# Kernel tuning notes

Measured on AMD Instinct MI355X. Metric: run time of the kernel, lower is better.

Reference implementation:

```python
import jax, jax.numpy as jnp
import numpy as np

HIDDEN = 1024
NUM_HEADS = 16
HEAD_DIM = HIDDEN // NUM_HEADS
ROPE_THETA = 10000.0


def rope_tables(seq_len, head_dim, theta):
    inv_freq = 1.0 / theta ** (jnp.arange(0, head_dim, 2, dtype=jnp.float32) / head_dim)
    pos = jnp.arange(seq_len, dtype=jnp.float32)
    freqs = jnp.outer(pos, inv_freq)  # [S, hd/2]
    return jnp.cos(freqs), jnp.sin(freqs)


def apply_rope(x, cos, sin):
    # x: [B, nh, S, hd]; cos/sin: [S, hd/2]
    x1, x2 = jnp.split(x, 2, axis=-1)
    return jnp.concatenate([x1 * cos - x2 * sin, x2 * cos + x1 * sin], axis=-1)


def setup_inputs() -> dict:
    key = jax.random.key(0)
    k1, k2, k3 = jax.random.split(key, 3)
    B, S = 2, 2048
    hidden_states = jax.random.normal(k1, (B, S, HIDDEN), dtype=jnp.float32)
    # nn.Linear stores weight as [out, in]; y = x @ W.T
    Wqkv = jax.random.normal(k2, (3 * HIDDEN, HIDDEN), dtype=jnp.float32) * (HIDDEN ** -0.5)
    Wo = jax.random.normal(k3, (HIDDEN, HIDDEN), dtype=jnp.float32) * (HIDDEN ** -0.5)
    return {"hidden_states": hidden_states, "Wqkv": Wqkv, "Wo": Wo}


def reference(hidden_states, Wqkv, Wo):
    B, S, H = hidden_states.shape
    qkv = hidden_states @ Wqkv.T  # [B, S, 3H]
    qkv = qkv.reshape(B, S, 3, NUM_HEADS, HEAD_DIM)
    q, k, v = jnp.moveaxis(qkv, 2, 0)  # each [B, S, nh, hd]
    q = jnp.transpose(q, (0, 2, 1, 3))  # [B, nh, S, hd]
    k = jnp.transpose(k, (0, 2, 1, 3))
    v = jnp.transpose(v, (0, 2, 1, 3))
    cos, sin = rope_tables(S, HEAD_DIM, ROPE_THETA)
    q = apply_rope(q, cos, sin)
    k = apply_rope(k, cos, sin)
    scale = 1.0 / jnp.sqrt(jnp.asarray(HEAD_DIM, dtype=q.dtype))
    scores = jnp.einsum("bhqd,bhkd->bhqk", q, k) * scale
    causal = jnp.tril(jnp.ones((S, S), dtype=bool))
    scores = jnp.where(causal, scores, jnp.finfo(scores.dtype).min)
    attn = jax.nn.softmax(scores, axis=-1)
    out = jnp.einsum("bhqk,bhkd->bhqd", attn, v)  # [B, nh, S, hd]
    out = jnp.transpose(out, (0, 2, 1, 3)).reshape(B, S, H)
    return out @ Wo.T
```

## Files before the change

kernel.cpp:

```cpp
#include <hip/hip_runtime.h>
#include <hip/hip_bf16.h>
#include <math.h>

typedef __bf16 bf16_t;
typedef __attribute__((ext_vector_type(8))) __bf16 bf16x8;
typedef __attribute__((ext_vector_type(4))) float f32x4;
typedef __attribute__((ext_vector_type(16))) float f32x16;
typedef __attribute__((ext_vector_type(4))) unsigned u32x4;

#define AS1(p) ((__attribute__((address_space(1))) void*)(p))
#define AS3(p) ((__attribute__((address_space(3))) void*)(p))

__device__ inline unsigned pkbf(float a, float b) {
  bf16_t x = (bf16_t)a, y = (bf16_t)b;
  return (unsigned)__builtin_bit_cast(unsigned short, x) |
         ((unsigned)__builtin_bit_cast(unsigned short, y) << 16);
}
__device__ inline f32x16 zero16() {
  f32x16 z;
#pragma unroll
  for (int r = 0; r < 16; ++r) z[r] = 0.f;
  return z;
}

__device__ inline void cvt8(const float* __restrict__ in, bf16_t* __restrict__ out, int i) {
  const float4* p = (const float4*)in;
  float4 a = p[2 * i], b = p[2 * i + 1];
  bf16x8 o;
  o[0] = (bf16_t)a.x; o[1] = (bf16_t)a.y; o[2] = (bf16_t)a.z; o[3] = (bf16_t)a.w;
  o[4] = (bf16_t)b.x; o[5] = (bf16_t)b.y; o[6] = (bf16_t)b.z; o[7] = (bf16_t)b.w;
  ((bf16x8*)out)[i] = o;
}

__global__ __launch_bounds__(256)
void prep_all(const float* __restrict__ hid, const float* __restrict__ wqkv,
              const float* __restrict__ wo, bf16_t* __restrict__ hidb,
              bf16_t* __restrict__ wqkvb, bf16_t* __restrict__ wob,
              float* __restrict__ cosb, float* __restrict__ sinb) {
  const int bid = blockIdx.x, tid = threadIdx.x;
  if (bid < 2048) {
    cvt8(hid, hidb, bid * 256 + tid);
  } else if (bid < 3584) {
    cvt8(wqkv, wqkvb, (bid - 2048) * 256 + tid);
  } else if (bid < 4096) {
    cvt8(wo, wob, (bid - 3584) * 256 + tid);
  } else {
    int t = (bid - 4096) * 256 + tid;
    int s = t >> 5, i = t & 31;
    float inv = powf(10000.0f, -(float)i / 32.0f);
    float sv, cv;
    sincosf((float)s * inv, &sv, &cv);
    cosb[t] = cv;
    sinb[t] = sv;
  }
}

#define GSTAGE32(KT, BUF)                                                                  \
  do {                                                                                     \
    const int k0_ = (KT) << 5;                                                             \
    const int ar_ = tid >> 2, ac_ = (tid & 3) * 8;                                         \
    __builtin_amdgcn_global_load_lds(AS1(A + (size_t)(m0 + ar_) * K + k0_ + ac_),          \
                                     AS3(&lA[BUF][ar_ * 32 + ac_]), 16, 0, 0);             \
    __builtin_amdgcn_global_load_lds(AS1(A + (size_t)(m0 + 64 + ar_) * K + k0_ + ac_),     \
                                     AS3(&lA[BUF][(64 + ar_) * 32 + ac_]), 16, 0, 0);      \
    __builtin_amdgcn_global_load_lds(AS1(B + (size_t)(n0 + ar_) * K + k0_ + ac_),          \
                                     AS3(&lB[BUF][ar_ * 32 + ac_]), 16, 0, 0);             \
    __builtin_amdgcn_global_load_lds(AS1(B + (size_t)(n0 + 64 + ar_) * K + k0_ + ac_),     \
                                     AS3(&lB[BUF][(64 + ar_) * 32 + ac_]), 16, 0, 0);      \
  } while (0)

__global__ __launch_bounds__(256, 3)
void gemm_qkv(const bf16_t* __restrict__ A, const bf16_t* __restrict__ B,
              bf16_t* __restrict__ qkv, bf16_t* __restrict__ Kp,
              const float* __restrict__ cosb, const float* __restrict__ sinb) {
  __shared__ __align__(16) bf16_t lA[3][128 * 32];
  __shared__ __align__(16) bf16_t lB[3][128 * 32];
  const int K = 1024;
  const int tid = threadIdx.x;
  const int wid = tid >> 6, lane = tid & 63;
  const int lr = lane & 15, lg = lane >> 4;
  const int nwg = gridDim.x * gridDim.y;
  int lin = blockIdx.y * gridDim.x + blockIdx.x;
  lin = (lin & 7) * (nwg >> 3) + (lin >> 3);
  const int m0 = (lin / gridDim.x) * 128, n0 = (lin % gridDim.x) * 128;
  const int wm = (wid >> 1) * 64, wn = (wid & 1) * 64;
  f32x4 acc[4][4];
#pragma unroll
  for (int i = 0; i < 4; ++i)
#pragma unroll
    for (int j = 0; j < 4; ++j) acc[i][j] = f32x4{0.f, 0.f, 0.f, 0.f};

  const int nk = 32;
  GSTAGE32(0, 0);
  GSTAGE32(1, 1);
  int cbuf = 0;
  for (int kt = 0; kt < nk; ++kt) {
    if (kt + 2 < nk) {
      const int sb = cbuf == 0 ? 2 : cbuf - 1;
      GSTAGE32(kt + 2, sb);
      asm volatile("s_waitcnt vmcnt(8)" ::: "memory");
    } else if (kt + 1 < nk) {
      asm volatile("s_waitcnt vmcnt(4)" ::: "memory");
    } else {
      asm volatile("s_waitcnt vmcnt(0)" ::: "memory");
    }
    __builtin_amdgcn_s_barrier();
    {
      bf16x8 af[4], bfr[4];
#pragma unroll
      for (int i = 0; i < 4; ++i) {
        af[i]  = *(const bf16x8*)&lA[cbuf][(wm + i * 16 + lr) * 32 + lg * 8];
        bfr[i] = *(const bf16x8*)&lB[cbuf][(wn + i * 16 + lr) * 32 + lg * 8];
      }
#pragma unroll
      for (int i = 0; i < 4; ++i)
#pragma unroll
        for (int j = 0; j < 4; ++j)
          acc[i][j] = __builtin_amdgcn_mfma_f32_16x16x32_bf16(af[i], bfr[j], acc[i][j], 0, 0, 0);
    }
    __builtin_amdgcn_s_barrier();
    cbuf = cbuf == 2 ? 0 : cbuf + 1;
  }
  const int sec = n0 >> 10;
  const int hcol = ((n0 + wn) & 1023) >> 6;
  if (sec == 2) {
#pragma unroll
    for (int i = 0; i < 4; ++i) {
      int token0 = m0 + wm + i * 16 + lg * 4;
      int bb = token0 >> 11;
      int t = (token0 & 2047) >> 6;
      int kv0 = token0 & 63;
      bf16_t* vd = qkv + ((size_t)(bb * 2048 + t * 64)) * 3072 + 2048 + hcol * 64;
#pragma unroll
      for (int j = 0; j < 4; ++j) {
        int d = j * 16 + lr;
        uint2 w;
        w.x = pkbf(acc[i][j][0], acc[i][j][1]);
        w.y = pkbf(acc[i][j][2], acc[i][j][3]);
        *(uint2*)(vd + (size_t)d * 3072 + (((kv0 >> 3) ^ (d & 7)) * 8) + (kv0 & 7)) = w;
      }
    }
  } else {
    const float SC = sec ? 1.0f : 0.125f * 1.4426950408889634f;
#pragma unroll
    for (int i = 0; i < 4; ++i)
#pragma unroll
      for (int r = 0; r < 4; ++r) {
        int token = m0 + wm + i * 16 + lg * 4 + r;
        int s = token & 2047;
#pragma unroll
        for (int j = 0; j < 2; ++j) {
          int f = j * 16 + lr;
          float cv = cosb[s * 32 + f], sv = sinb[s * 32 + f];
          float x1 = acc[i][j][r], x2 = acc[i][j + 2][r];
          float y1 = (x1 * cv - x2 * sv) * SC;
          float y2 = (x2 * cv + x1 * sv) * SC;
          if (sec == 0) {
            bf16_t* qd = qkv + (size_t)token * 3072 + hcol * 64;
            qd[f] = (bf16_t)y1;
            qd[f + 32] = (bf16_t)y2;
          } else {
            int bb = token >> 11, t = (token & 2047) >> 6, rk = token & 63;
            bf16_t* kd = Kp + ((size_t)((bb * 16 + hcol) * 32 + t)) * 4096 + rk * 64;
            int c1 = f >> 3;
            kd[((c1 ^ (rk & 7)) * 8) + (lr & 7)] = (bf16_t)y1;
            kd[(((c1 + 4) ^ (rk & 7)) * 8) + (lr & 7)] = (bf16_t)y2;
          }
        }
      }
  }
}

__global__ __launch_bounds__(256, 3)
void gemm_nt_f32(const bf16_t* __restrict__ A, const bf16_t* __restrict__ B,
                 float* __restrict__ C, int M, int N, int K) {
  __shared__ __align__(16) bf16_t lA[3][128 * 32];
  __shared__ __align__(16) bf16_t lB[3][128 * 32];
  const int tid = threadIdx.x;
  const int wid = tid >> 6, lane = tid & 63;
  const int lr = lane & 15, lg = lane >> 4;
  const int nwg = gridDim.x * gridDim.y;
  int lin = blockIdx.y * gridDim.x + blockIdx.x;
  lin = (lin & 7) * (nwg >> 3) + (lin >> 3);
  const int m0 = (lin / gridDim.x) * 128, n0 = (lin % gridDim.x) * 128;
  const int wm = (wid >> 1) * 64, wn = (wid & 1) * 64;
  f32x4 acc[4][4];
#pragma unroll
  for (int i = 0; i < 4; ++i)
#pragma unroll
    for (int j = 0; j < 4; ++j) acc[i][j] = f32x4{0.f, 0.f, 0.f, 0.f};

  const int nk = K >> 5;
  GSTAGE32(0, 0);
  GSTAGE32(1, 1);
  int cbuf = 0;
  for (int kt = 0; kt < nk; ++kt) {
    if (kt + 2 < nk) {
      const int sb = cbuf == 0 ? 2 : cbuf - 1;
      GSTAGE32(kt + 2, sb);
      asm volatile("s_waitcnt vmcnt(8)" ::: "memory");
    } else if (kt + 1 < nk) {
      asm volatile("s_waitcnt vmcnt(4)" ::: "memory");
    } else {
      asm volatile("s_waitcnt vmcnt(0)" ::: "memory");
    }
    __builtin_amdgcn_s_barrier();
    {
      bf16x8 af[4], bfr[4];
#pragma unroll
      for (int i = 0; i < 4; ++i) {
        af[i]  = *(const bf16x8*)&lA[cbuf][(wm + i * 16 + lr) * 32 + lg * 8];
        bfr[i] = *(const bf16x8*)&lB[cbuf][(wn + i * 16 + lr) * 32 + lg * 8];
      }
#pragma unroll
      for (int i = 0; i < 4; ++i)
#pragma unroll
        for (int j = 0; j < 4; ++j)
          acc[i][j] = __builtin_amdgcn_mfma_f32_16x16x32_bf16(af[i], bfr[j], acc[i][j], 0, 0, 0);
    }
    __builtin_amdgcn_s_barrier();
    cbuf = cbuf == 2 ? 0 : cbuf + 1;
  }
#pragma unroll
  for (int i = 0; i < 4; ++i)
#pragma unroll
    for (int j = 0; j < 4; ++j)
#pragma unroll
      for (int r = 0; r < 4; ++r) {
        int row = m0 + wm + i * 16 + lg * 4 + r;
        int col = n0 + wn + j * 16 + lr;
        C[(size_t)row * N + col] = acc[i][j][r];
      }
}

__device__ const unsigned char ROLE_LUT[44] = {
    19, 18, 17, 16,
    15, 95, 159, 158,
    14, 94, 93, 157,
    13, 92, 156, 91, 155, 154,
    12, 90, 89, 153, 152,
    11, 88, 87, 151, 150,
    10, 86, 85, 149, 148,
    9, 84,
    8, 7, 6, 5, 4, 3, 2, 1, 0};

__global__ __launch_bounds__(128, 2)
void attn_fwd(const bf16_t* __restrict__ qkv, const bf16_t* __restrict__ Kp,
              bf16_t* __restrict__ O, bf16_t* __restrict__ Po, float* __restrict__ Plp) {
  __shared__ __align__(16) bf16_t Ksh[2][4096];
  __shared__ __align__(16) bf16_t Vsh[2][4096];
  const int tid = threadIdx.x, wid = tid >> 6, lane = tid & 63;
  const int ln = lane & 31, h = lane >> 5;
  const int lin = blockIdx.x;
  const int e = ROLE_LUT[lin >> 5];
  const int bh = lin & 31;
  const int c = e & 31, kind = e >> 6;
  const int b = bh >> 4, hd = bh & 15;
  const int t0 = (kind == 2) ? ((c + 1) >> 1) : 0;
  const int t1 = (kind == 1) ? ((c + 1) >> 1) : c + 1;
  const int qw = c * 64 + wid * 32;

  const bf16_t* Qrow = qkv + ((size_t)(b * 2048 + qw + ln)) * 3072 + hd * 64;
  bf16x8 qf[4];
#pragma unroll
  for (int t = 0; t < 4; ++t) qf[t] = *(const bf16x8*)(Qrow + t * 16 + h * 8);

  f32x16 o0 = zero16(), o1 = zero16();
  float lp = 0.f;

  const bf16_t* Kbase = Kp + ((size_t)bh * 32) * 4096 + tid * 8;
  const bf16_t* Vbase = qkv + ((size_t)(b * 2048 + (tid >> 3))) * 3072 + 2048 + hd * 64 + (tid & 7) * 8;

#define STAGE(T, BUF)                                                                     \
  do {                                                                                    \
    const bf16_t* ks = Kbase + (size_t)(T) * 4096;                                        \
    __builtin_amdgcn_global_load_lds(AS1(ks),        AS3(&Ksh[BUF][tid * 8]), 16, 0, 0);  \
    __builtin_amdgcn_global_load_lds(AS1(ks + 1024), AS3(&Ksh[BUF][1024 + tid * 8]), 16, 0, 0); \
    __builtin_amdgcn_global_load_lds(AS1(ks + 2048), AS3(&Ksh[BUF][2048 + tid * 8]), 16, 0, 0); \
    __builtin_amdgcn_global_load_lds(AS1(ks + 3072), AS3(&Ksh[BUF][3072 + tid * 8]), 16, 0, 0); \
    const bf16_t* vs = Vbase + (size_t)(T) * 64 * 3072;                                   \
    __builtin_amdgcn_global_load_lds(AS1(vs),             AS3(&Vsh[BUF][tid * 8]), 16, 0, 0);        \
    __builtin_amdgcn_global_load_lds(AS1(vs + 16 * 3072), AS3(&Vsh[BUF][1024 + tid * 8]), 16, 0, 0); \
    __builtin_amdgcn_global_load_lds(AS1(vs + 32 * 3072), AS3(&Vsh[BUF][2048 + tid * 8]), 16, 0, 0); \
    __builtin_amdgcn_global_load_lds(AS1(vs + 48 * 3072), AS3(&Vsh[BUF][3072 + tid * 8]), 16, 0, 0); \
  } while (0)

  STAGE(t0, t0 & 1);
  for (int t = t0; t < t1; ++t) {
    asm volatile("s_waitcnt vmcnt(0)" ::: "memory");
    __builtin_amdgcn_s_barrier();
    if (t + 1 < t1) STAGE(t + 1, (t + 1) & 1);
    const bf16_t* K = &Ksh[t & 1][0];
    const bf16_t* V = &Vsh[t & 1][0];
    f32x16 s0 = zero16(), s1 = zero16();
    __builtin_amdgcn_s_setprio(1);
#pragma unroll
    for (int u = 0; u < 4; ++u) {
      const int ch = 2 * u + h;
      bf16x8 k0 = *(const bf16x8*)&K[ln * 64 + ((ch ^ (ln & 7)) * 8)];
      bf16x8 k1 = *(const bf16x8*)&K[(32 + ln) * 64 + ((ch ^ (ln & 7)) * 8)];
      s0 = __builtin_amdgcn_mfma_f32_32x32x16_bf16(k0, qf[u], s0, 0, 0, 0);
      s1 = __builtin_amdgcn_mfma_f32_32x32x16_bf16(k1, qf[u], s1, 0, 0, 0);
    }
    __builtin_amdgcn_s_setprio(0);
    if (t == c) {
      const int qg = qw + ln, k0g = t * 64;
#pragma unroll
      for (int r = 0; r < 16; ++r) {
        int kv = k0g + (r & 3) + 8 * (r >> 2) + 4 * h;
        if (kv > qg) s0[r] = -3e38f;
        if (kv + 32 > qg) s1[r] = -3e38f;
      }
    }
#pragma unroll
    for (int r = 0; r < 16; ++r) {
      float p0 = __builtin_amdgcn_exp2f(s0[r]); lp += p0; s0[r] = p0;
      float p1 = __builtin_amdgcn_exp2f(s1[r]); lp += p1; s1[r] = p1;
    }
    __builtin_amdgcn_s_setprio(1);
#pragma unroll
    for (int u = 0; u < 4; ++u) {
      const int w = u & 1;
      f32x16 sv = (u >> 1) ? s1 : s0;
      unsigned x  = pkbf(sv[8 * w + 0], sv[8 * w + 1]);
      unsigned x2 = pkbf(sv[8 * w + 2], sv[8 * w + 3]);
      unsigned y  = pkbf(sv[8 * w + 4], sv[8 * w + 5]);
      unsigned y2 = pkbf(sv[8 * w + 6], sv[8 * w + 7]);
      asm volatile("v_permlane32_swap_b32 %0, %1" : "+v"(x), "+v"(y));
      asm volatile("v_permlane32_swap_b32 %0, %1" : "+v"(x2), "+v"(y2));
      u32x4 pw; pw[0] = x; pw[1] = x2; pw[2] = y; pw[3] = y2;
      bf16x8 pf = __builtin_bit_cast(bf16x8, pw);
      const int ch = 2 * u + h;
      bf16x8 v0 = *(const bf16x8*)&V[ln * 64 + ((ch ^ (ln & 7)) * 8)];
      bf16x8 v1 = *(const bf16x8*)&V[(32 + ln) * 64 + ((ch ^ (ln & 7)) * 8)];
      o0 = __builtin_amdgcn_mfma_f32_32x32x16_bf16(v0, pf, o0, 0, 0, 0);
      o1 = __builtin_amdgcn_mfma_f32_32x32x16_bf16(v1, pf, o1, 0, 0, 0);
    }
    __builtin_amdgcn_s_setprio(0);
  }
#undef STAGE
  float lpf = lp + __shfl_xor(lp, 32, 64);
  if (kind == 0) {
    float inv = 1.0f / lpf;
    bf16_t* Oaddr = O + ((size_t)(b * 2048 + qw + ln)) * 1024 + hd * 64;
#pragma unroll
    for (int D = 0; D < 2; ++D) {
      f32x16 ov = D ? o1 : o0;
#pragma unroll
      for (int Q = 0; Q < 4; ++Q) {
        uint2 w;
        w.x = pkbf(ov[4 * Q + 0] * inv, ov[4 * Q + 1] * inv);
        w.y = pkbf(ov[4 * Q + 2] * inv, ov[4 * Q + 3] * inv);
        *(uint2*)(Oaddr + D * 32 + Q * 8 + 4 * h) = w;
      }
    }
  } else {
    const int slot = (bh * 12 + (c - 20)) * 2 + (kind - 1);
    const int qi = wid * 32 + ln;
    if (h == 0) Plp[slot * 64 + qi] = lpf;
    bf16_t* Paddr = Po + ((size_t)(slot * 64 + qi)) * 64;
#pragma unroll
    for (int D = 0; D < 2; ++D) {
      f32x16 ov = D ? o1 : o0;
#pragma unroll
      for (int Q = 0; Q < 4; ++Q) {
        uint2 w;
        w.x = pkbf(ov[4 * Q + 0], ov[4 * Q + 1]);
        w.y = pkbf(ov[4 * Q + 2], ov[4 * Q + 3]);
        *(uint2*)(Paddr + D * 32 + Q * 8 + 4 * h) = w;
      }
    }
  }
}

__global__ __launch_bounds__(64)
void attn_combine(const bf16_t* __restrict__ Po, const float* __restrict__ Plp,
                  bf16_t* __restrict__ O) {
  const int blk = blockIdx.x;
  const int bh = blk / 12, sc = blk % 12;
  const int b = bh >> 4, hd = bh & 15;
  const int c = 20 + sc;
  const int q = threadIdx.x;
  const int slotA = (bh * 12 + sc) * 2, slotB = slotA + 1;
  float inv = 1.0f / (Plp[slotA * 64 + q] + Plp[slotB * 64 + q]);
  const bf16x8* pa = (const bf16x8*)(Po + ((size_t)(slotA * 64 + q)) * 64);
  const bf16x8* pb = (const bf16x8*)(Po + ((size_t)(slotB * 64 + q)) * 64);
  bf16_t* oaddr = O + ((size_t)(b * 2048 + c * 64 + q)) * 1024 + hd * 64;
#pragma unroll
  for (int j = 0; j < 8; ++j) {
    bf16x8 a = pa[j], v = pb[j];
    bf16x8 w;
#pragma unroll
    for (int k = 0; k < 8; ++k) w[k] = (bf16_t)(((float)a[k] + (float)v[k]) * inv);
    ((bf16x8*)oaddr)[j] = w;
  }
}

extern "C" void kernel_launch(void* const* d_in, const int* in_sizes, int n_in,
                              void* d_out, int out_size, void* d_ws, size_t ws_size,
                              hipStream_t stream) {
  const float* hid  = (const float*)d_in[0];
  const float* wqkv = (const float*)d_in[1];
  const float* wo   = (const float*)d_in[2];
  float* out = (float*)d_out;
  char* ws = (char*)d_ws;
  bf16_t* hidb  = (bf16_t*)(ws);
  bf16_t* wqkvb = (bf16_t*)(ws + 8388608);
  bf16_t* wob   = (bf16_t*)(ws + 14680064);
  bf16_t* qkvb  = (bf16_t*)(ws + 16777216);
  float*  cosb  = (float*)(ws + 41943040);
  float*  sinb  = (float*)(ws + 42205184);
  bf16_t* Ob    = (bf16_t*)(ws + 42467328);
  bf16_t* Kp    = (bf16_t*)(ws + 52428800);
  bf16_t* Po    = (bf16_t*)(ws + 60817408);
  float*  Plp   = (float*)(ws + 67108864);

  prep_all<<<4352, 256, 0, stream>>>(hid, wqkv, wo, hidb, wqkvb, wob, cosb, sinb);
  gemm_qkv<<<dim3(24, 32), 256, 0, stream>>>(hidb, wqkvb, qkvb, Kp, cosb, sinb);
  attn_fwd<<<1408, 128, 0, stream>>>(qkvb, Kp, Ob, Po, Plp);
  attn_combine<<<384, 64, 0, stream>>>(Po, Plp, Ob);
  gemm_nt_f32<<<dim3(8, 32), 256, 0, stream>>>(Ob, wob, out, 4096, 1024, 1024);
}
```

Before: 114.5 us.

## Rewrite QKV GEMM with 256x256 tiles, 8 waves, swizzled LDS, phased pipeline

```diff
diff --git a/kernel.cpp b/kernel.cpp
--- a/kernel.cpp
+++ b/kernel.cpp
@@ -55,77 +55,135 @@
   }
 }
 
-#define GSTAGE32(KT, BUF)                                                                  \
-  do {                                                                                     \
-    const int k0_ = (KT) << 5;                                                             \
-    const int ar_ = tid >> 2, ac_ = (tid & 3) * 8;                                         \
-    __builtin_amdgcn_global_load_lds(AS1(A + (size_t)(m0 + ar_) * K + k0_ + ac_),          \
-                                     AS3(&lA[BUF][ar_ * 32 + ac_]), 16, 0, 0);             \
-    __builtin_amdgcn_global_load_lds(AS1(A + (size_t)(m0 + 64 + ar_) * K + k0_ + ac_),     \
-                                     AS3(&lA[BUF][(64 + ar_) * 32 + ac_]), 16, 0, 0);      \
-    __builtin_amdgcn_global_load_lds(AS1(B + (size_t)(n0 + ar_) * K + k0_ + ac_),          \
-                                     AS3(&lB[BUF][ar_ * 32 + ac_]), 16, 0, 0);             \
-    __builtin_amdgcn_global_load_lds(AS1(B + (size_t)(n0 + 64 + ar_) * K + k0_ + ac_),     \
-                                     AS3(&lB[BUF][(64 + ar_) * 32 + ac_]), 16, 0, 0);      \
-  } while (0)
-
-__global__ __launch_bounds__(256, 3)
+__global__ __launch_bounds__(512, 2)
 void gemm_qkv(const bf16_t* __restrict__ A, const bf16_t* __restrict__ B,
               bf16_t* __restrict__ qkv, bf16_t* __restrict__ Kp,
               const float* __restrict__ cosb, const float* __restrict__ sinb) {
-  __shared__ __align__(16) bf16_t lA[3][128 * 32];
-  __shared__ __align__(16) bf16_t lB[3][128 * 32];
+  __shared__ __align__(16) bf16_t smem[65536];
   const int K = 1024;
   const int tid = threadIdx.x;
   const int wid = tid >> 6, lane = tid & 63;
   const int lr = lane & 15, lg = lane >> 4;
-  const int nwg = gridDim.x * gridDim.y;
-  int lin = blockIdx.y * gridDim.x + blockIdx.x;
-  lin = (lin & 7) * (nwg >> 3) + (lin >> 3);
-  const int m0 = (lin / gridDim.x) * 128, n0 = (lin % gridDim.x) * 128;
-  const int wm = (wid >> 1) * 64, wn = (wid & 1) * 64;
-  f32x4 acc[4][4];
-#pragma unroll
-  for (int i = 0; i < 4; ++i)
+  int orig = blockIdx.x;
+  int wg = (orig & 7) * 24 + (orig >> 3);
+  const int m0 = (wg % 16) * 256, n0 = (wg / 16) * 256;
+  const int wm = (wid >> 2) * 128;
+  const int wn = (wid & 3) * 64;
+  const bf16_t* Asrc = A + (size_t)m0 * K;
+  const bf16_t* Bsrc = B + (size_t)n0 * K;
+
+  f32x4 acc[8][4];
+#pragma unroll
+  for (int i = 0; i < 8; ++i)
 #pragma unroll
     for (int j = 0; j < 4; ++j) acc[i][j] = f32x4{0.f, 0.f, 0.f, 0.f};
 
-  const int nk = 32;
-  GSTAGE32(0, 0);
-  GSTAGE32(1, 1);
-  int cbuf = 0;
-  for (int kt = 0; kt < nk; ++kt) {
-    if (kt + 2 < nk) {
-      const int sb = cbuf == 0 ? 2 : cbuf - 1;
-      GSTAGE32(kt + 2, sb);
-      asm volatile("s_waitcnt vmcnt(8)" ::: "memory");
-    } else if (kt + 1 < nk) {
-      asm volatile("s_waitcnt vmcnt(4)" ::: "memory");
-    } else {
-      asm volatile("s_waitcnt vmcnt(0)" ::: "memory");
-    }
-    __builtin_amdgcn_s_barrier();
-    {
-      bf16x8 af[4], bfr[4];
-#pragma unroll
-      for (int i = 0; i < 4; ++i) {
-        af[i]  = *(const bf16x8*)&lA[cbuf][(wm + i * 16 + lr) * 32 + lg * 8];
-        bfr[i] = *(const bf16x8*)&lB[cbuf][(wn + i * 16 + lr) * 32 + lg * 8];
-      }
-#pragma unroll
-      for (int i = 0; i < 4; ++i)
-#pragma unroll
-        for (int j = 0; j < 4; ++j)
-          acc[i][j] = __builtin_amdgcn_mfma_f32_16x16x32_bf16(af[i], bfr[j], acc[i][j], 0, 0, 0);
-    }
-    __builtin_amdgcn_s_barrier();
-    cbuf = cbuf == 2 ? 0 : cbuf + 1;
-  }
+  auto stageHalf = [&](const bf16_t* src, int T, int reg, int h, int c) {
+#pragma unroll
+    for (int l = 0; l < 2; ++l) {
+      int dl = h * 16384 + l * 8192 + tid * 16;
+      int s = dl ^ (((dl >> 9) & 3) << 5);
+      int row = s >> 7, colb = s & 127;
+      __builtin_amdgcn_global_load_lds(
+          AS1(src + (size_t)row * K + T * 64 + (colb >> 1)),
+          AS3((char*)smem + c * 65536 + reg * 32768 + dl), 16, 0, 0);
+    }
+  };
+  auto rd = [&](int c, int reg, int row, int ks) -> bf16x8 {
+    int b = row * 128 + ks * 64 + lg * 16;
+    b ^= ((b >> 9) & 3) << 5;
+    return *(const bf16x8*)((const char*)smem + c * 65536 + reg * 32768 + b);
+  };
+
+#define PHASE_TAIL(Q)                                                            \
+  __builtin_amdgcn_s_barrier();                                                  \
+  asm volatile("s_waitcnt lgkmcnt(0)" ::: "memory");                             \
+  __builtin_amdgcn_sched_barrier(0);                                             \
+  __builtin_amdgcn_s_setprio(1);                                                 \
+  _Pragma("unroll") for (int ii = 0; ii < 2; ++ii)                               \
+  _Pragma("unroll") for (int j = 0; j < 4; ++j)                                  \
+  _Pragma("unroll") for (int ks = 0; ks < 2; ++ks)                               \
+      acc[2 * (Q) + ii][j] = __builtin_amdgcn_mfma_f32_16x16x32_bf16(            \
+          af[ii][ks], bf[j][ks], acc[2 * (Q) + ii][j], 0, 0, 0);                 \
+  __builtin_amdgcn_s_setprio(0);                                                 \
+  __builtin_amdgcn_s_barrier();
+
+  stageHalf(Bsrc, 0, 1, 0, 0); stageHalf(Bsrc, 0, 1, 1, 0);
+  stageHalf(Asrc, 0, 0, 0, 0); stageHalf(Asrc, 0, 0, 1, 0);
+  stageHalf(Bsrc, 1, 1, 0, 1); stageHalf(Bsrc, 1, 1, 1, 1);
+  asm volatile("s_waitcnt vmcnt(4)" ::: "memory");
+  __builtin_amdgcn_s_barrier();
+
+  for (int it = 0; it < 8; ++it) {
+    const int t = 2 * it;
+    bf16x8 bf[4][2], af[2][2];
+#pragma unroll
+    for (int j = 0; j < 4; ++j)
+#pragma unroll
+      for (int ks = 0; ks < 2; ++ks) bf[j][ks] = rd(0, 1, wn + j * 16 + lr, ks);
+#pragma unroll
+    for (int ii = 0; ii < 2; ++ii)
+#pragma unroll
+      for (int ks = 0; ks < 2; ++ks) af[ii][ks] = rd(0, 0, wm + ii * 16 + lr, ks);
+    stageHalf(Asrc, t + 1, 0, 0, 1);
+    stageHalf(Asrc, t + 1, 0, 1, 1);
+    PHASE_TAIL(0)
+#pragma unroll
+    for (int ii = 0; ii < 2; ++ii)
+#pragma unroll
+      for (int ks = 0; ks < 2; ++ks) af[ii][ks] = rd(0, 0, wm + (2 + ii) * 16 + lr, ks);
+    if (it < 7) stageHalf(Bsrc, t + 2, 1, 0, 0);
+    PHASE_TAIL(1)
+#pragma unroll
+    for (int ii = 0; ii < 2; ++ii)
+#pragma unroll
+      for (int ks = 0; ks < 2; ++ks) af[ii][ks] = rd(0, 0, wm + (4 + ii) * 16 + lr, ks);
+    if (it < 7) stageHalf(Bsrc, t + 2, 1, 1, 0);
+    PHASE_TAIL(2)
+#pragma unroll
+    for (int ii = 0; ii < 2; ++ii)
+#pragma unroll
+      for (int ks = 0; ks < 2; ++ks) af[ii][ks] = rd(0, 0, wm + (6 + ii) * 16 + lr, ks);
+    if (it < 7) { asm volatile("s_waitcnt vmcnt(4)" ::: "memory"); }
+    else        { asm volatile("s_waitcnt vmcnt(0)" ::: "memory"); }
+    PHASE_TAIL(3)
+#pragma unroll
+    for (int j = 0; j < 4; ++j)
+#pragma unroll
+      for (int ks = 0; ks < 2; ++ks) bf[j][ks] = rd(1, 1, wn + j * 16 + lr, ks);
+#pragma unroll
+    for (int ii = 0; ii < 2; ++ii)
+#pragma unroll
+      for (int ks = 0; ks < 2; ++ks) af[ii][ks] = rd(1, 0, wm + ii * 16 + lr, ks);
+    if (it < 7) { stageHalf(Asrc, t + 2, 0, 0, 0); stageHalf(Asrc, t + 2, 0, 1, 0); }
+    PHASE_TAIL(0)
+#pragma unroll
+    for (int ii = 0; ii < 2; ++ii)
+#pragma unroll
+      for (int ks = 0; ks < 2; ++ks) af[ii][ks] = rd(1, 0, wm + (2 + ii) * 16 + lr, ks);
+    if (it < 7) stageHalf(Bsrc, t + 3, 1, 0, 1);
+    PHASE_TAIL(1)
+#pragma unroll
+    for (int ii = 0; ii < 2; ++ii)
+#pragma unroll
+      for (int ks = 0; ks < 2; ++ks) af[ii][ks] = rd(1, 0, wm + (4 + ii) * 16 + lr, ks);
+    if (it < 7) stageHalf(Bsrc, t + 3, 1, 1, 1);
+    PHASE_TAIL(2)
+#pragma unroll
+    for (int ii = 0; ii < 2; ++ii)
+#pragma unroll
+      for (int ks = 0; ks < 2; ++ks) af[ii][ks] = rd(1, 0, wm + (6 + ii) * 16 + lr, ks);
+    if (it < 7) { asm volatile("s_waitcnt vmcnt(4)" ::: "memory"); }
+    else        { asm volatile("s_waitcnt vmcnt(0)" ::: "memory"); }
+    PHASE_TAIL(3)
+  }
+#undef PHASE_TAIL
+
   const int sec = n0 >> 10;
   const int hcol = ((n0 + wn) & 1023) >> 6;
   if (sec == 2) {
 #pragma unroll
-    for (int i = 0; i < 4; ++i) {
+    for (int i = 0; i < 8; ++i) {
       int token0 = m0 + wm + i * 16 + lg * 4;
       int bb = token0 >> 11;
       int t = (token0 & 2047) >> 6;
@@ -143,7 +201,7 @@
   } else {
     const float SC = sec ? 1.0f : 0.125f * 1.4426950408889634f;
 #pragma unroll
-    for (int i = 0; i < 4; ++i)
+    for (int i = 0; i < 8; ++i)
 #pragma unroll
       for (int r = 0; r < 4; ++r) {
         int token = m0 + wm + i * 16 + lg * 4 + r;
@@ -171,6 +229,20 @@
   }
 }
 
+#define GSTAGE32(KT, BUF)                                                                  \
+  do {                                                                                     \
+    const int k0_ = (KT) << 5;                                                             \
+    const int ar_ = tid >> 2, ac_ = (tid & 3) * 8;                                         \
+    __builtin_amdgcn_global_load_lds(AS1(A + (size_t)(m0 + ar_) * K + k0_ + ac_),          \
+                                     AS3(&lA[BUF][ar_ * 32 + ac_]), 16, 0, 0);             \
+    __builtin_amdgcn_global_load_lds(AS1(A + (size_t)(m0 + 64 + ar_) * K + k0_ + ac_),     \
+                                     AS3(&lA[BUF][(64 + ar_) * 32 + ac_]), 16, 0, 0);      \
+    __builtin_amdgcn_global_load_lds(AS1(B + (size_t)(n0 + ar_) * K + k0_ + ac_),          \
+                                     AS3(&lB[BUF][ar_ * 32 + ac_]), 16, 0, 0);             \
+    __builtin_amdgcn_global_load_lds(AS1(B + (size_t)(n0 + 64 + ar_) * K + k0_ + ac_),     \
+                                     AS3(&lB[BUF][(64 + ar_) * 32 + ac_]), 16, 0, 0);      \
+  } while (0)
+
 __global__ __launch_bounds__(256, 3)
 void gemm_nt_f32(const bf16_t* __restrict__ A, const bf16_t* __restrict__ B,
                  float* __restrict__ C, int M, int N, int K) {
@@ -416,7 +488,7 @@
   float*  Plp   = (float*)(ws + 67108864);
 
   prep_all<<<4352, 256, 0, stream>>>(hid, wqkv, wo, hidb, wqkvb, wob, cosb, sinb);
-  gemm_qkv<<<dim3(24, 32), 256, 0, stream>>>(hidb, wqkvb, qkvb, Kp, cosb, sinb);
+  gemm_qkv<<<192, 512, 0, stream>>>(hidb, wqkvb, qkvb, Kp, cosb, sinb);
   attn_fwd<<<1408, 128, 0, stream>>>(qkvb, Kp, Ob, Po, Plp);
   attn_combine<<<384, 64, 0, stream>>>(Po, Plp, Ob);
   gemm_nt_f32<<<dim3(8, 32), 256, 0, stream>>>(Ob, wob, out, 4096, 1024, 1024);
```

New measurement: 122.4 us. 1.07x slower.

## Split KV tiles across two wave pairs in attention and merge partials via LDS

Applied to the files above, without the earlier changes.

```diff
diff --git a/kernel.cpp b/kernel.cpp
--- a/kernel.cpp
+++ b/kernel.cpp
@@ -244,13 +244,14 @@
     9, 84,
     8, 7, 6, 5, 4, 3, 2, 1, 0};
 
-__global__ __launch_bounds__(128, 2)
+__global__ __launch_bounds__(256, 2)
 void attn_fwd(const bf16_t* __restrict__ qkv, const bf16_t* __restrict__ Kp,
               bf16_t* __restrict__ O, bf16_t* __restrict__ Po, float* __restrict__ Plp) {
-  __shared__ __align__(16) bf16_t Ksh[2][4096];
-  __shared__ __align__(16) bf16_t Vsh[2][4096];
+  __shared__ __align__(16) bf16_t Ksh[2][2][4096];
+  __shared__ __align__(16) bf16_t Vsh[2][2][4096];
   const int tid = threadIdx.x, wid = tid >> 6, lane = tid & 63;
   const int ln = lane & 31, h = lane >> 5;
+  const int pid = wid >> 1, qh = wid & 1;
   const int lin = blockIdx.x;
   const int e = ROLE_LUT[lin >> 5];
   const int bh = lin & 31;
@@ -258,7 +259,8 @@
   const int b = bh >> 4, hd = bh & 15;
   const int t0 = (kind == 2) ? ((c + 1) >> 1) : 0;
   const int t1 = (kind == 1) ? ((c + 1) >> 1) : c + 1;
-  const int qw = c * 64 + wid * 32;
+  const int S = (t1 - t0 + 1) >> 1;
+  const int qw = c * 64 + qh * 32;
 
   const bf16_t* Qrow = qkv + ((size_t)(b * 2048 + qw + ln)) * 3072 + hd * 64;
   bf16x8 qf[4];
@@ -271,74 +273,107 @@
   const bf16_t* Kbase = Kp + ((size_t)bh * 32) * 4096 + tid * 8;
   const bf16_t* Vbase = qkv + ((size_t)(b * 2048 + (tid >> 3))) * 3072 + 2048 + hd * 64 + (tid & 7) * 8;
 
-#define STAGE(T, BUF)                                                                     \
-  do {                                                                                    \
-    const bf16_t* ks = Kbase + (size_t)(T) * 4096;                                        \
-    __builtin_amdgcn_global_load_lds(AS1(ks),        AS3(&Ksh[BUF][tid * 8]), 16, 0, 0);  \
-    __builtin_amdgcn_global_load_lds(AS1(ks + 1024), AS3(&Ksh[BUF][1024 + tid * 8]), 16, 0, 0); \
-    __builtin_amdgcn_global_load_lds(AS1(ks + 2048), AS3(&Ksh[BUF][2048 + tid * 8]), 16, 0, 0); \
-    __builtin_amdgcn_global_load_lds(AS1(ks + 3072), AS3(&Ksh[BUF][3072 + tid * 8]), 16, 0, 0); \
-    const bf16_t* vs = Vbase + (size_t)(T) * 64 * 3072;                                   \
-    __builtin_amdgcn_global_load_lds(AS1(vs),             AS3(&Vsh[BUF][tid * 8]), 16, 0, 0);        \
-    __builtin_amdgcn_global_load_lds(AS1(vs + 16 * 3072), AS3(&Vsh[BUF][1024 + tid * 8]), 16, 0, 0); \
-    __builtin_amdgcn_global_load_lds(AS1(vs + 32 * 3072), AS3(&Vsh[BUF][2048 + tid * 8]), 16, 0, 0); \
-    __builtin_amdgcn_global_load_lds(AS1(vs + 48 * 3072), AS3(&Vsh[BUF][3072 + tid * 8]), 16, 0, 0); \
+#define STAGE2(I, SSET)                                                                    \
+  do {                                                                                     \
+    _Pragma("unroll")                                                                      \
+    for (int tl_ = 0; tl_ < 2; ++tl_) {                                                    \
+      int tt_ = t0 + 2 * (I) + tl_;                                                        \
+      if (tt_ < t1) {                                                                      \
+        const bf16_t* ks_ = Kbase + (size_t)tt_ * 4096;                                    \
+        __builtin_amdgcn_global_load_lds(AS1(ks_), AS3(&Ksh[SSET][tl_][tid * 8]), 16, 0, 0); \
+        __builtin_amdgcn_global_load_lds(AS1(ks_ + 2048),                                  \
+                                         AS3(&Ksh[SSET][tl_][2048 + tid * 8]), 16, 0, 0);  \
+        const bf16_t* vs_ = Vbase + (size_t)tt_ * 64 * 3072;                               \
+        __builtin_amdgcn_global_load_lds(AS1(vs_), AS3(&Vsh[SSET][tl_][tid * 8]), 16, 0, 0); \
+        __builtin_amdgcn_global_load_lds(AS1(vs_ + (size_t)32 * 3072),                     \
+                                         AS3(&Vsh[SSET][tl_][2048 + tid * 8]), 16, 0, 0);  \
+      }                                                                                    \
+    }                                                                                      \
   } while (0)
 
-  STAGE(t0, t0 & 1);
-  for (int t = t0; t < t1; ++t) {
-    asm volatile("s_waitcnt vmcnt(0)" ::: "memory");
-    __builtin_amdgcn_s_barrier();
-    if (t + 1 < t1) STAGE(t + 1, (t + 1) & 1);
-    const bf16_t* K = &Ksh[t & 1][0];
-    const bf16_t* V = &Vsh[t & 1][0];
-    f32x16 s0 = zero16(), s1 = zero16();
-    __builtin_amdgcn_s_setprio(1);
-#pragma unroll
-    for (int u = 0; u < 4; ++u) {
-      const int ch = 2 * u + h;
-      bf16x8 k0 = *(const bf16x8*)&K[ln * 64 + ((ch ^ (ln & 7)) * 8)];
-      bf16x8 k1 = *(const bf16x8*)&K[(32 + ln) * 64 + ((ch ^ (ln & 7)) * 8)];
-      s0 = __builtin_amdgcn_mfma_f32_32x32x16_bf16(k0, qf[u], s0, 0, 0, 0);
-      s1 = __builtin_amdgcn_mfma_f32_32x32x16_bf16(k1, qf[u], s1, 0, 0, 0);
-    }
-    __builtin_amdgcn_s_setprio(0);
-    if (t == c) {
-      const int qg = qw + ln, k0g = t * 64;
+  STAGE2(0, 0);
+  for (int i = 0; i < S; ++i) {
+    const int nnext = (i + 1 < S) ? ((t1 - t0 - 2 * (i + 1)) >= 2 ? 2 : 1) : 0;
+    if (nnext) STAGE2(i + 1, (i + 1) & 1);
+    if (nnext == 2)      { asm volatile("s_waitcnt vmcnt(8)" ::: "memory"); }
+    else if (nnext == 1) { asm volatile("s_waitcnt vmcnt(4)" ::: "memory"); }
+    else                 { asm volatile("s_waitcnt vmcnt(0)" ::: "memory"); }
+    __builtin_amdgcn_s_barrier();
+    const int t = t0 + 2 * i + pid;
+    if (t < t1) {
+      const bf16_t* K = &Ksh[i & 1][pid][0];
+      const bf16_t* V = &Vsh[i & 1][pid][0];
+      f32x16 s0 = zero16(), s1 = zero16();
+      __builtin_amdgcn_s_setprio(1);
+#pragma unroll
+      for (int u = 0; u < 4; ++u) {
+        const int ch = 2 * u + h;
+        bf16x8 k0 = *(const bf16x8*)&K[ln * 64 + ((ch ^ (ln & 7)) * 8)];
+        bf16x8 k1 = *(const bf16x8*)&K[(32 + ln) * 64 + ((ch ^ (ln & 7)) * 8)];
+        s0 = __builtin_amdgcn_mfma_f32_32x32x16_bf16(k0, qf[u], s0, 0, 0, 0);
+        s1 = __builtin_amdgcn_mfma_f32_32x32x16_bf16(k1, qf[u], s1, 0, 0, 0);
+      }
+      __builtin_amdgcn_s_setprio(0);
+      if (t == c) {
+        const int qg = qw + ln, k0g = t * 64;
+#pragma unroll
+        for (int r = 0; r < 16; ++r) {
+          int kv = k0g + (r & 3) + 8 * (r >> 2) + 4 * h;
+          if (kv > qg) s0[r] = -3e38f;
+          if (kv + 32 > qg) s1[r] = -3e38f;
+        }
+      }
 #pragma unroll
       for (int r = 0; r < 16; ++r) {
-        int kv = k0g + (r & 3) + 8 * (r >> 2) + 4 * h;
-        if (kv > qg) s0[r] = -3e38f;
-        if (kv + 32 > qg) s1[r] = -3e38f;
-      }
-    }
+        float p0 = __builtin_amdgcn_exp2f(s0[r]); lp += p0; s0[r] = p0;
+        float p1 = __builtin_amdgcn_exp2f(s1[r]); lp += p1; s1[r] = p1;
+      }
+      __builtin_amdgcn_s_setprio(1);
+#pragma unroll
+      for (int u = 0; u < 4; ++u) {
+        const int w = u & 1;
+        f32x16 sv = (u >> 1) ? s1 : s0;
+        unsigned x  = pkbf(sv[8 * w + 0], sv[8 * w + 1]);
+        unsigned x2 = pkbf(sv[8 * w + 2], sv[8 * w + 3]);
+        unsigned y  = pkbf(sv[8 * w + 4], sv[8 * w + 5]);
+        unsigned y2 = pkbf(sv[8 * w + 6], sv[8 * w + 7]);
+        asm volatile("v_permlane32_swap_b32 %0, %1" : "+v"(x), "+v"(y));
+        asm volatile("v_permlane32_swap_b32 %0, %1" : "+v"(x2), "+v"(y2));
+        u32x4 pw; pw[0] = x; pw[1] = x2; pw[2] = y; pw[3] = y2;
+        bf16x8 pf = __builtin_bit_cast(bf16x8, pw);
+        const int ch = 2 * u + h;
+        bf16x8 v0 = *(const bf16x8*)&V[ln * 64 + ((ch ^ (ln & 7)) * 8)];
+        bf16x8 v1 = *(const bf16x8*)&V[(32 + ln) * 64 + ((ch ^ (ln & 7)) * 8)];
+        o0 = __builtin_amdgcn_mfma_f32_32x32x16_bf16(v0, pf, o0, 0, 0, 0);
+        o1 = __builtin_amdgcn_mfma_f32_32x32x16_bf16(v1, pf, o1, 0, 0, 0);
+      }
+      __builtin_amdgcn_s_setprio(0);
+    }
+    __builtin_amdgcn_s_barrier();
+  }
+#undef STAGE2
+  {
+    float* ob  = (float*)&Ksh[0][0][0];
+    float* lpb = (float*)&Vsh[0][0][0];
+    if (pid == 1) {
+      const int idx = qh * 64 + lane;
+#pragma unroll
+      for (int r = 0; r < 16; ++r) {
+        ob[idx * 32 + r] = o0[r];
+        ob[idx * 32 + 16 + r] = o1[r];
+      }
+      lpb[idx] = lp;
+    }
+    __syncthreads();
+    if (pid == 1) return;
+    const int idx = qh * 64 + lane;
 #pragma unroll
     for (int r = 0; r < 16; ++r) {
-      float p0 = __builtin_amdgcn_exp2f(s0[r]); lp += p0; s0[r] = p0;
-      float p1 = __builtin_amdgcn_exp2f(s1[r]); lp += p1; s1[r] = p1;
-    }
-    __builtin_amdgcn_s_setprio(1);
-#pragma unroll
-    for (int u = 0; u < 4; ++u) {
-      const int w = u & 1;
-      f32x16 sv = (u >> 1) ? s1 : s0;
-      unsigned x  = pkbf(sv[8 * w + 0], sv[8 * w + 1]);
-      unsigned x2 = pkbf(sv[8 * w + 2], sv[8 * w + 3]);
-      unsigned y  = pkbf(sv[8 * w + 4], sv[8 * w + 5]);
-      unsigned y2 = pkbf(sv[8 * w + 6], sv[8 * w + 7]);
-      asm volatile("v_permlane32_swap_b32 %0, %1" : "+v"(x), "+v"(y));
-      asm volatile("v_permlane32_swap_b32 %0, %1" : "+v"(x2), "+v"(y2));
-      u32x4 pw; pw[0] = x; pw[1] = x2; pw[2] = y; pw[3] = y2;
-      bf16x8 pf = __builtin_bit_cast(bf16x8, pw);
-      const int ch = 2 * u + h;
-      bf16x8 v0 = *(const bf16x8*)&V[ln * 64 + ((ch ^ (ln & 7)) * 8)];
-      bf16x8 v1 = *(const bf16x8*)&V[(32 + ln) * 64 + ((ch ^ (ln & 7)) * 8)];
-      o0 = __builtin_amdgcn_mfma_f32_32x32x16_bf16(v0, pf, o0, 0, 0, 0);
-      o1 = __builtin_amdgcn_mfma_f32_32x32x16_bf16(v1, pf, o1, 0, 0, 0);
-    }
-    __builtin_amdgcn_s_setprio(0);
-  }
-#undef STAGE
+      o0[r] += ob[idx * 32 + r];
+      o1[r] += ob[idx * 32 + 16 + r];
+    }
+    lp += lpb[idx];
+  }
   float lpf = lp + __shfl_xor(lp, 32, 64);
   if (kind == 0) {
     float inv = 1.0f / lpf;
@@ -356,7 +391,7 @@
     }
   } else {
     const int slot = (bh * 12 + (c - 20)) * 2 + (kind - 1);
-    const int qi = wid * 32 + ln;
+    const int qi = qh * 32 + ln;
     if (h == 0) Plp[slot * 64 + qi] = lpf;
     bf16_t* Paddr = Po + ((size_t)(slot * 64 + qi)) * 64;
 #pragma unroll
@@ -417,7 +452,7 @@
 
   prep_all<<<4352, 256, 0, stream>>>(hid, wqkv, wo, hidb, wqkvb, wob, cosb, sinb);
   gemm_qkv<<<dim3(24, 32), 256, 0, stream>>>(hidb, wqkvb, qkvb, Kp, cosb, sinb);
-  attn_fwd<<<1408, 128, 0, stream>>>(qkvb, Kp, Ob, Po, Plp);
+  attn_fwd<<<1408, 256, 0, stream>>>(qkvb, Kp, Ob, Po, Plp);
   attn_combine<<<384, 64, 0, stream>>>(Po, Plp, Ob);
   gemm_nt_f32<<<dim3(8, 32), 256, 0, stream>>>(Ob, wob, out, 4096, 1024, 1024);
 }
```

New measurement: 115.2 us. About the same (+0.7%).
